# Kernel optimization log

Hardware: AMD Instinct MI355X
Metric: run time of the kernel (lower is better)

Reference implementation:

```python
import jax
import jax.numpy as jnp
from jax import lax
import numpy as np

IN_CH, HID, GROUPS = 1024, 256, 8
B, H, W = 16, 64, 64
CPG = HID // GROUPS  # channels per group = 32
EPS = 1e-5


def setup_inputs() -> dict:
    key = jax.random.key(0)
    ks = jax.random.split(key, 8)
    s = 0.02  # small init scale so activations stay well-behaved
    return {
        "x": jax.random.normal(ks[0], (B, IN_CH, H, W), jnp.float32),
        "ctx_w": jax.random.normal(ks[1], (HID, IN_CH), jnp.float32) * s,
        "ctx_b": jnp.zeros((HID,), jnp.float32),
        "kg_w1": jax.random.normal(ks[2], (2 * HID, HID), jnp.float32) * s,
        "kg_b1": jnp.zeros((2 * HID,), jnp.float32),
        "kg_w2": jax.random.normal(ks[3], (GROUPS * 9, 2 * HID), jnp.float32) * s,
        "kg_b2": jnp.zeros((GROUPS * 9,), jnp.float32),
        "in_w": jax.random.normal(ks[4], (HID, IN_CH), jnp.float32) * s,
        "in_b": jnp.zeros((HID,), jnp.float32),
        "out_w": jax.random.normal(ks[5], (HID, HID), jnp.float32) * s,
        "out_b": jnp.zeros((HID,), jnp.float32),
        "gamma": jnp.ones((HID,), jnp.float32),
        "beta": jnp.zeros((HID,), jnp.float32),
    }


def reference(x, ctx_w, ctx_b, kg_w1, kg_b1, kg_w2, kg_b2,
              in_w, in_b, out_w, out_b, gamma, beta):
    b = x.shape[0]
    # context pooling: global avg pool -> 1x1 conv -> relu
    ctx = jnp.mean(x, axis=(2, 3))                       # [B, C_in]
    ctx = jax.nn.relu(ctx @ ctx_w.T + ctx_b)             # [B, HID]
    # kernel generator MLP -> per-sample per-group 3x3 kernels
    hddn = jax.nn.relu(ctx @ kg_w1.T + kg_b1)            # [B, 2*HID]
    kernels = (hddn @ kg_w2.T + kg_b2).reshape(b, GROUPS, 3, 3)
    # input transform (1x1 conv)
    xt = jnp.einsum('bchw,oc->bohw', x, in_w) + in_b[None, :, None, None]
    # expand group kernels to per-channel depthwise kernels [B, HID, 3, 3]
    kch = jnp.repeat(kernels, CPG, axis=1)
    # per-sample depthwise 3x3 conv, padding=1
    def dwconv(xi, ki):  # xi: [HID, H, W], ki: [HID, 3, 3]
        return lax.conv_general_dilated(
            xi[None], ki[:, None], window_strides=(1, 1), padding='SAME',
            dimension_numbers=('NCHW', 'OIHW', 'NCHW'),
            feature_group_count=HID)[0]
    out = jax.vmap(dwconv)(xt, kch)                      # [B, HID, H, W]
    # output transform (1x1 conv)
    out = jnp.einsum('bchw,oc->bohw', out, out_w) + out_b[None, :, None, None]
    # BatchNorm2d (training-mode batch statistics)
    mean = jnp.mean(out, axis=(0, 2, 3))
    var = jnp.var(out, axis=(0, 2, 3))
    out = gamma[None, :, None, None] * (out - mean[None, :, None, None]) \
          * lax.rsqrt(var[None, :, None, None] + EPS) + beta[None, :, None, None]
    return xt + out
```

## Files before the change

kernel.cpp:

```cpp
#include <hip/hip_runtime.h>

#define BATCH 16
#define CIN   1024
#define HID   256
#define HW    4096

typedef __attribute__((ext_vector_type(8))) short bf16x8;
typedef __attribute__((ext_vector_type(4))) float f32x4;

struct __align__(16) f4  { float v[4]; };
struct __align__(8)  us4 { unsigned short v[4]; };
struct __align__(16) us8 { unsigned short v[8]; };

__device__ __forceinline__ float bf2f(unsigned short u) {
  unsigned int x = ((unsigned int)u) << 16;
  return __builtin_bit_cast(float, x);
}
__device__ __forceinline__ unsigned short f2bf(float f) {
  unsigned int u = __builtin_bit_cast(unsigned int, f);
  u += 0x7fff + ((u >> 16) & 1);
  return (unsigned short)(u >> 16);
}

#define LGWB() do { __builtin_amdgcn_sched_barrier(0); \
  asm volatile("s_waitcnt lgkmcnt(0)" ::: "memory"); \
  __builtin_amdgcn_s_barrier(); \
  __builtin_amdgcn_sched_barrier(0); } while (0)

__global__ __launch_bounds__(256)
void prep_kernel(const float* __restrict__ A1, unsigned short* __restrict__ O1,
                 const float* __restrict__ A2, unsigned short* __restrict__ O2,
                 float* __restrict__ zbuf)
{
  const int bidx = blockIdx.x;
  if (bidx >= 160) {
    int idx = (bidx - 160) * 256 + threadIdx.x;
    if (idx < 16896) zbuf[idx] = 0.f;
    return;
  }
  const float* A; unsigned short* O; int KD, u;
  if (bidx < 128) { A = A1; O = O1; KD = 1024; u = bidx * 256 + threadIdx.x; }
  else            { A = A2; O = O2; KD = 256;  u = (bidx - 128) * 256 + threadIdx.x; }
  const int t    = u >> 11;
  const int r    = u & 2047;
  const int wm   = r >> 9, kk = (r >> 8) & 1, mi = (r >> 6) & 3, lane = r & 63;
  const int row  = wm * 64 + mi * 16 + (lane & 15);
  const int k    = t * 64 + kk * 32 + (lane >> 4) * 8;
  f4 v0 = *(const f4*)(A + (size_t)row * KD + k);
  f4 v1 = *(const f4*)(A + (size_t)row * KD + k + 4);
  us8 w = { f2bf(v0.v[0]), f2bf(v0.v[1]), f2bf(v0.v[2]), f2bf(v0.v[3]),
            f2bf(v1.v[0]), f2bf(v1.v[1]), f2bf(v1.v[2]), f2bf(v1.v[3]) };
  *(us8*)(O + (size_t)u * 8) = w;
}

__global__ __launch_bounds__(512, 2)
void gemm1_kernel(const unsigned short* __restrict__ Afrag, const float* __restrict__ xb,
                  const float* __restrict__ bias, unsigned short* __restrict__ Cout,
                  float* __restrict__ ctx_sum)
{
  constexpr int NT = 16;
  __shared__ unsigned short B_sh[2][128 * 64];
  __shared__ float ctx_lds[1024];

  const int tid  = threadIdx.x;
  const int lane = tid & 63;
  const int wv   = tid >> 6;
  const int wm   = wv >> 1, wn = wv & 1;
  const int lr   = lane & 15, lg = lane >> 4;
  const int hi   = lane >> 5, q = lane & 31;

  const int b    = blockIdx.x >> 5;
  const int pix0 = (blockIdx.x & 31) << 7;

  for (int i = tid; i < 1024; i += 512) ctx_lds[i] = 0.f;
  __syncthreads();

  f32x4 acc[4][4] = {};
  const size_t rowbase = ((size_t)b * CIN + 8 * wv + hi) * HW + pix0 + 4 * q;
  const char*  abase   = (const char*)Afrag + wm * 8192 + lane * 16;

  bf16x8 aA[8], aB[8];
  f4 rfA[4], rfB[4];

  auto ISSUE_A = [&](int t, bf16x8* a) {
    const char* p = abase + t * 32768;
    #pragma unroll
    for (int i = 0; i < 8; ++i) a[i] = *(const bf16x8*)(p + i * 1024);
  };
  auto LOADB = [&](int t, f4* rf) {
    const float* p = xb + rowbase + (size_t)t * 64 * HW;
    #pragma unroll
    for (int i = 0; i < 4; ++i) rf[i] = *(const f4*)(p + (size_t)(2 * i) * HW);
  };
  auto WRITEB = [&](int sel, int t, f4* rf) {
    #pragma unroll
    for (int i = 0; i < 4; ++i) {
      float s = rf[i].v[0] + rf[i].v[1] + rf[i].v[2] + rf[i].v[3];
      #pragma unroll
      for (int m = 1; m < 32; m <<= 1) s += __shfl_xor(s, m, 64);
      if (q == 0) atomicAdd(&ctx_lds[t * 64 + 8 * wv + 2 * i + hi], s);
    }
    unsigned int u[4][2];
    #pragma unroll
    for (int i = 0; i < 4; ++i) {
      asm("v_cvt_pk_bf16_f32 %0, %1, %2" : "=v"(u[i][0]) : "v"(rf[i].v[0]), "v"(rf[i].v[1]));
      asm("v_cvt_pk_bf16_f32 %0, %1, %2" : "=v"(u[i][1]) : "v"(rf[i].v[2]), "v"(rf[i].v[3]));
    }
    unsigned int w[4][2];
    #pragma unroll
    for (int i = 0; i < 4; ++i) {
      w[i][0] = __shfl_xor(u[i][0], 32, 64);
      w[i][1] = __shfl_xor(u[i][1], 32, 64);
    }
    #pragma unroll
    for (int jj = 0; jj < 2; ++jj) {
      unsigned int A0 = hi ? w[2][jj] : u[0][jj];
      unsigned int A1 = hi ? u[2][jj] : w[0][jj];
      unsigned int A2 = hi ? w[3][jj] : u[1][jj];
      unsigned int A3 = hi ? u[3][jj] : w[1][jj];
      #pragma unroll
      for (int sub = 0; sub < 2; ++sub) {
        unsigned int lo, h2;
        if (sub == 0) { lo = (A0 & 0xffffu) | (A1 << 16);  h2 = (A2 & 0xffffu) | (A3 << 16); }
        else          { lo = (A0 >> 16) | (A1 & 0xffff0000u); h2 = (A2 >> 16) | (A3 & 0xffff0000u); }
        int p  = 4 * q + jj * 2 + sub;
        int fx = ((p >> 2) ^ p) & 7;
        int byte = p * 128 + (((wv ^ fx) & 7) << 4) + hi * 8;
        uint2 val; val.x = lo; val.y = h2;
        *(uint2*)((char*)B_sh[sel] + byte) = val;
      }
    }
  };
  auto COMPUTE = [&](int sel, bf16x8* a) {
    #pragma unroll
    for (int kk = 0; kk < 2; ++kk) {
      bf16x8 bfr[4];
      #pragma unroll
      for (int ni = 0; ni < 4; ++ni) {
        int pr = wn * 64 + ni * 16 + lr;
        int fx = ((pr >> 2) ^ pr) & 7;
        int byte = pr * 128 + ((((kk * 4 + lg) ^ fx) & 7) << 4);
        bfr[ni] = *(const bf16x8*)((const char*)B_sh[sel] + byte);
      }
      #pragma unroll
      for (int mi = 0; mi < 4; ++mi)
        #pragma unroll
        for (int ni = 0; ni < 4; ++ni)
          acc[mi][ni] = __builtin_amdgcn_mfma_f32_16x16x32_bf16(a[kk * 4 + mi], bfr[ni], acc[mi][ni], 0, 0, 0);
    }
  };

  ISSUE_A(0, aA);
  LOADB(0, rfA);
  LOADB(1, rfB);

  #pragma unroll
  for (int t = 0; t < NT; t += 2) {
    WRITEB(0, t, rfA);
    ISSUE_A(t + 1, aB);
    __builtin_amdgcn_sched_barrier(0);
    if (t + 2 < NT) LOADB(t + 2, rfA);
    LGWB();
    COMPUTE(0, aA);
    WRITEB(1, t + 1, rfB);
    if (t + 2 < NT) ISSUE_A(t + 2, aA);
    __builtin_amdgcn_sched_barrier(0);
    if (t + 3 < NT) LOADB(t + 3, rfB);
    LGWB();
    COMPUTE(1, aB);
  }

  #pragma unroll
  for (int mi = 0; mi < 4; ++mi) {
    #pragma unroll
    for (int r = 0; r < 4; ++r) {
      int o = wm * 64 + mi * 16 + lg * 4 + r;
      float bo = bias[o];
      #pragma unroll
      for (int ni = 0; ni < 4; ++ni) {
        int pix = pix0 + wn * 64 + ni * 16 + lr;
        Cout[((size_t)(b * HID + o)) * HW + pix] = f2bf(acc[mi][ni][r] + bo);
      }
    }
  }
  __syncthreads();
  for (int e = tid; e < 1024; e += 512)
    atomicAdd(&ctx_sum[(size_t)b * 1024 + e], ctx_lds[e]);
}

__global__ __launch_bounds__(512, 2)
void gemm2_fused_kernel(const unsigned short* __restrict__ Afrag,
                        const unsigned short* __restrict__ xt,
                        const float* __restrict__ kern, const float* __restrict__ bias,
                        unsigned short* __restrict__ Cout, float* __restrict__ bn_sums)
{
  constexpr int NT = 4;
  __shared__ unsigned short B_sh[128 * 64];
  __shared__ unsigned short xs[64 * 260];
  __shared__ float kf_s[72];
  __shared__ float bn_lds[512];

  const int tid  = threadIdx.x;
  const int lane = tid & 63;
  const int wv   = tid >> 6;
  const int wm   = wv >> 1, wn = wv & 1;
  const int lr   = lane & 15, lg = lane >> 4;

  const int b    = blockIdx.x >> 5;
  const int R    = blockIdx.x & 31;
  const int pix0 = R << 7;
  const int g0   = R << 1;

  if (tid < 512) bn_lds[tid] = 0.f;
  if (tid < 72)  kf_s[tid] = kern[b * 72 + tid];
  __syncthreads();

  f32x4 acc[4][4] = {};
  const int c4 = tid & 15, q = tid >> 4;
  const int prow  = q >> 4;
  const int pcol4 = (q & 15) << 2;
  const int grp9  = (c4 >> 3) * 9;

  const char* abase = (const char*)Afrag + wm * 8192 + lane * 16;

  bf16x8 aA[8];
  us8 rx[4];

  auto PREXS = [&](int t) {
    #pragma unroll
    for (int it = 0; it < 4; ++it) {
      int flat = it * 512 + tid;
      int ch = flat >> 5, r4 = (flat >> 3) & 3, c8 = flat & 7;
      int grow = g0 - 1 + r4;
      if ((unsigned)grow < 64u) {
        rx[it] = *(const us8*)(xt + ((size_t)(b * HID + t * 64 + ch) << 12) + grow * 64 + c8 * 8);
      } else {
        us8 z = {0, 0, 0, 0, 0, 0, 0, 0}; rx[it] = z;
      }
    }
  };
  auto WRXS = [&]() {
    #pragma unroll
    for (int it = 0; it < 4; ++it) {
      int flat = it * 512 + tid;
      int ch = flat >> 5, r4 = (flat >> 3) & 3, c8 = flat & 7;
      int o = ch * 260 + r4 * 64 + c8 * 8;
      *(us4*)(xs + o)     = *(const us4*)(&rx[it].v[0]);
      *(us4*)(xs + o + 4) = *(const us4*)(&rx[it].v[4]);
    }
  };
  auto ISSUE_A = [&](int t) {
    const char* p = abase + t * 32768;
    #pragma unroll
    for (int i = 0; i < 8; ++i) aA[i] = *(const bf16x8*)(p + i * 1024);
  };

  PREXS(0);
  ISSUE_A(0);

  for (int t = 0; t < NT; ++t) {
    WRXS();
    __syncthreads();
    if (t + 1 < NT) PREXS(t + 1);
    {
      const float k0 = kf_s[2 * t * 9 + grp9 + 0], k1 = kf_s[2 * t * 9 + grp9 + 1], k2 = kf_s[2 * t * 9 + grp9 + 2];
      const float k3 = kf_s[2 * t * 9 + grp9 + 3], k4 = kf_s[2 * t * 9 + grp9 + 4], k5 = kf_s[2 * t * 9 + grp9 + 5];
      const float k6 = kf_s[2 * t * 9 + grp9 + 6], k7 = kf_s[2 * t * 9 + grp9 + 7], k8 = kf_s[2 * t * 9 + grp9 + 8];
      float dwv[4][4];
      #pragma unroll
      for (int i = 0; i < 4; ++i) {
        int ch = 4 * c4 + i;
        #pragma unroll
        for (int j = 0; j < 4; ++j) dwv[i][j] = 0.f;
        #pragma unroll
        for (int ky = 0; ky < 3; ++ky) {
          int ro = ch * 260 + (prow + ky) * 64;
          float v[6];
          unsigned int p0 = (pcol4 > 0)  ? *(const unsigned int*)(xs + ro + pcol4 - 2) : 0u;
          unsigned int p1 = *(const unsigned int*)(xs + ro + pcol4);
          unsigned int p2 = *(const unsigned int*)(xs + ro + pcol4 + 2);
          unsigned int p3 = (pcol4 < 60) ? *(const unsigned int*)(xs + ro + pcol4 + 4) : 0u;
          v[0] = bf2f((unsigned short)(p0 >> 16));
          v[1] = bf2f((unsigned short)(p1 & 0xffff));
          v[2] = bf2f((unsigned short)(p1 >> 16));
          v[3] = bf2f((unsigned short)(p2 & 0xffff));
          v[4] = bf2f((unsigned short)(p2 >> 16));
          v[5] = bf2f((unsigned short)(p3 & 0xffff));
          float ka = (ky == 0) ? k0 : (ky == 1) ? k3 : k6;
          float kb = (ky == 0) ? k1 : (ky == 1) ? k4 : k7;
          float kc = (ky == 0) ? k2 : (ky == 1) ? k5 : k8;
          #pragma unroll
          for (int j = 0; j < 4; ++j)
            dwv[i][j] += v[j] * ka + v[j + 1] * kb + v[j + 2] * kc;
        }
      }
      #pragma unroll
      for (int j = 0; j < 4; ++j) {
        int pix = 4 * q + j;
        us4 w = { f2bf(dwv[0][j]), f2bf(dwv[1][j]), f2bf(dwv[2][j]), f2bf(dwv[3][j]) };
        *(us4*)((char*)B_sh + pix * 128 + ((8 * c4) ^ ((pix & 7) << 4))) = w;
      }
    }
    __syncthreads();
    #pragma unroll
    for (int kk = 0; kk < 2; ++kk) {
      bf16x8 bfr[4];
      #pragma unroll
      for (int ni = 0; ni < 4; ++ni) {
        int pr = wn * 64 + ni * 16 + lr;
        bfr[ni] = *(const bf16x8*)((const char*)B_sh + pr * 128 + ((((kk << 2) | lg) ^ (pr & 7)) << 4));
      }
      #pragma unroll
      for (int mi = 0; mi < 4; ++mi)
        #pragma unroll
        for (int ni = 0; ni < 4; ++ni)
          acc[mi][ni] = __builtin_amdgcn_mfma_f32_16x16x32_bf16(aA[kk * 4 + mi], bfr[ni], acc[mi][ni], 0, 0, 0);
    }
    if (t + 1 < NT) ISSUE_A(t + 1);
  }

  #pragma unroll
  for (int mi = 0; mi < 4; ++mi) {
    #pragma unroll
    for (int r = 0; r < 4; ++r) {
      int o = wm * 64 + mi * 16 + lg * 4 + r;
      float bo = bias[o];
      float s = 0.f, s2 = 0.f;
      #pragma unroll
      for (int ni = 0; ni < 4; ++ni) {
        int pix = pix0 + wn * 64 + ni * 16 + lr;
        float val = acc[mi][ni][r] + bo;
        Cout[((size_t)(b * HID + o)) * HW + pix] = f2bf(val);
        s += val; s2 += val * val;
      }
      #pragma unroll
      for (int msk = 1; msk < 16; msk <<= 1) {
        s  += __shfl_xor(s,  msk, 64);
        s2 += __shfl_xor(s2, msk, 64);
      }
      if (lr == 0) { atomicAdd(&bn_lds[o], s); atomicAdd(&bn_lds[256 + o], s2); }
    }
  }
  __syncthreads();
  if (tid < 512) atomicAdd(&bn_sums[tid], bn_lds[tid]);
}

template<int K, int N, bool RELU>
__global__ __launch_bounds__(256)
void fc_kernel(const float* __restrict__ in, const float* __restrict__ w,
               const float* __restrict__ bias, float* __restrict__ out, float scale)
{
  const int wid  = (blockIdx.x << 2) | (threadIdx.x >> 6);
  const int lane = threadIdx.x & 63;
  const int b = wid / N, o = wid - b * N;
  const float* ip = in + (size_t)b * K;
  const float* wp = w  + (size_t)o * K;
  float p = 0.f;
  #pragma unroll
  for (int k = 0; k < K / 64; ++k) p += ip[lane + k * 64] * wp[lane + k * 64];
  #pragma unroll
  for (int m = 1; m < 64; m <<= 1) p += __shfl_xor(p, m, 64);
  if (lane == 0) {
    float v = p * scale + bias[o];
    out[(size_t)b * N + o] = RELU ? fmaxf(v, 0.f) : v;
  }
}

__global__ __launch_bounds__(256)
void final_kernel(const unsigned short* __restrict__ xt, const unsigned short* __restrict__ ot,
                  const float* __restrict__ bn_sums, const float* __restrict__ gamma,
                  const float* __restrict__ beta, float* __restrict__ out)
{
  __shared__ float sc_s[256], sh_s[256];
  {
    int t = threadIdx.x;
    const float inv_n = 1.f / 65536.f;
    float m  = bn_sums[t] * inv_n;
    float v  = bn_sums[256 + t] * inv_n - m * m;
    float sc = gamma[t] * rsqrtf(v + 1e-5f);
    sc_s[t] = sc;
    sh_s[t] = beta[t] - m * sc;
  }
  __syncthreads();
  int g = blockIdx.x * 256 + threadIdx.x;
  const int stride = 4096 * 256;
  #pragma unroll
  for (int it = 0; it < 4; ++it, g += stride) {
    int o = (g >> 10) & 255;
    us4 a = ((const us4*)xt)[g];
    us4 c = ((const us4*)ot)[g];
    float s = sc_s[o], h = sh_s[o];
    f4 r;
    #pragma unroll
    for (int j = 0; j < 4; ++j) r.v[j] = bf2f(a.v[j]) + s * bf2f(c.v[j]) + h;
    *(f4*)(out + (size_t)g * 4) = r;
  }
}

extern "C" void kernel_launch(void* const* d_in, const int* in_sizes, int n_in,
                              void* d_out, int out_size, void* d_ws, size_t ws_size,
                              hipStream_t stream)
{
  const float* x     = (const float*)d_in[0];
  const float* ctx_w = (const float*)d_in[1];
  const float* ctx_b = (const float*)d_in[2];
  const float* kg_w1 = (const float*)d_in[3];
  const float* kg_b1 = (const float*)d_in[4];
  const float* kg_w2 = (const float*)d_in[5];
  const float* kg_b2 = (const float*)d_in[6];
  const float* in_w  = (const float*)d_in[7];
  const float* in_b  = (const float*)d_in[8];
  const float* out_w = (const float*)d_in[9];
  const float* out_b = (const float*)d_in[10];
  const float* gamma = (const float*)d_in[11];
  const float* beta  = (const float*)d_in[12];
  float* out = (float*)d_out;

  char* ws = (char*)d_ws;
  unsigned short* xt = (unsigned short*)ws;
  unsigned short* ot = (unsigned short*)(ws + 33554432);
  float* ctx_sum = (float*)(ws + 67108864);
  float* bn_sums = ctx_sum + 16384;
  float* kern    = bn_sums + 512;
  float* ctxbuf  = kern + 1152;
  float* hddnbuf = ctxbuf + 4096;
  unsigned short* afrag1 = (unsigned short*)(ws + 67108864 + 131072);
  unsigned short* afrag2 = (unsigned short*)(ws + 67108864 + 131072 + 524288);

  prep_kernel<<<226, 256, 0, stream>>>(in_w, afrag1, out_w, afrag2, ctx_sum);
  gemm1_kernel<<<512, 512, 0, stream>>>(afrag1, x, in_b, xt, ctx_sum);
  fc_kernel<1024, 256, true ><<<1024, 256, 0, stream>>>(ctx_sum, ctx_w, ctx_b, ctxbuf, 1.f / 4096.f);
  fc_kernel< 256, 512, true ><<<2048, 256, 0, stream>>>(ctxbuf,  kg_w1, kg_b1, hddnbuf, 1.f);
  fc_kernel< 512,  72, false><<< 288, 256, 0, stream>>>(hddnbuf, kg_w2, kg_b2, kern,    1.f);
  gemm2_fused_kernel<<<512, 512, 0, stream>>>(afrag2, xt, kern, out_b, ot, bn_sums);
  final_kernel<<<4096, 256, 0, stream>>>(xt, ot, bn_sums, gamma, beta, out);
}
```

Measured before the change: 165.0 us.

## Deepen gemm1 prefetch, lighten gemm2 barriers, fuse kernel-generator MLP launches

gemm1 now cycles three register buffers for x tiles, so each tile is loaded three steps ahead instead of two. The loop is fully unrolled through a STEP helper that alternates the A-fragment and LDS buffers. In gemm2, the two __syncthreads per iteration are replaced by the LGWB macro, a scheduled wait-plus-barrier, so outstanding loads can overlap the barrier better. The two kernel-generator fc launches are merged into one kg_kernel with one block per sample and the hidden layer kept in LDS. This removes a launch and an intermediate buffer, but the fused stage now runs on only 16 blocks and uses more registers.

```diff
diff --git a/kernel.cpp b/kernel.cpp
--- a/kernel.cpp
+++ b/kernel.cpp
@@ -80,7 +80,7 @@
   const char*  abase   = (const char*)Afrag + wm * 8192 + lane * 16;
 
   bf16x8 aA[8], aB[8];
-  f4 rfA[4], rfB[4];
+  f4 rfA[4], rfB[4], rfC[4];
 
   auto ISSUE_A = [&](int t, bf16x8* a) {
     const char* p = abase + t * 32768;
@@ -149,26 +149,26 @@
           acc[mi][ni] = __builtin_amdgcn_mfma_f32_16x16x32_bf16(a[kk * 4 + mi], bfr[ni], acc[mi][ni], 0, 0, 0);
     }
   };
+  auto STEP = [&](int t, f4* rfc, bf16x8* ac, bf16x8* an) {
+    WRITEB(t & 1, t, rfc);
+    if (t + 1 < NT) ISSUE_A(t + 1, an);
+    __builtin_amdgcn_sched_barrier(0);
+    if (t + 3 < NT) LOADB(t + 3, rfc);
+    LGWB();
+    COMPUTE(t & 1, ac);
+  };
 
   ISSUE_A(0, aA);
   LOADB(0, rfA);
   LOADB(1, rfB);
-
-  #pragma unroll
-  for (int t = 0; t < NT; t += 2) {
-    WRITEB(0, t, rfA);
-    ISSUE_A(t + 1, aB);
-    __builtin_amdgcn_sched_barrier(0);
-    if (t + 2 < NT) LOADB(t + 2, rfA);
-    LGWB();
-    COMPUTE(0, aA);
-    WRITEB(1, t + 1, rfB);
-    if (t + 2 < NT) ISSUE_A(t + 2, aA);
-    __builtin_amdgcn_sched_barrier(0);
-    if (t + 3 < NT) LOADB(t + 3, rfB);
-    LGWB();
-    COMPUTE(1, aB);
-  }
+  LOADB(2, rfC);
+
+  STEP( 0, rfA, aA, aB);  STEP( 1, rfB, aB, aA);  STEP( 2, rfC, aA, aB);
+  STEP( 3, rfA, aB, aA);  STEP( 4, rfB, aA, aB);  STEP( 5, rfC, aB, aA);
+  STEP( 6, rfA, aA, aB);  STEP( 7, rfB, aB, aA);  STEP( 8, rfC, aA, aB);
+  STEP( 9, rfA, aB, aA);  STEP(10, rfB, aA, aB);  STEP(11, rfC, aB, aA);
+  STEP(12, rfA, aA, aB);  STEP(13, rfB, aB, aA);  STEP(14, rfC, aA, aB);
+  STEP(15, rfA, aB, aA);
 
   #pragma unroll
   for (int mi = 0; mi < 4; ++mi) {
@@ -260,7 +260,7 @@
 
   for (int t = 0; t < NT; ++t) {
     WRXS();
-    __syncthreads();
+    LGWB();
     if (t + 1 < NT) PREXS(t + 1);
     {
       const float k0 = kf_s[2 * t * 9 + grp9 + 0], k1 = kf_s[2 * t * 9 + grp9 + 1], k2 = kf_s[2 * t * 9 + grp9 + 2];
@@ -301,7 +301,7 @@
         *(us4*)((char*)B_sh + pix * 128 + ((8 * c4) ^ ((pix & 7) << 4))) = w;
       }
     }
-    __syncthreads();
+    LGWB();
     #pragma unroll
     for (int kk = 0; kk < 2; ++kk) {
       bf16x8 bfr[4];
@@ -363,6 +363,38 @@
   if (lane == 0) {
     float v = p * scale + bias[o];
     out[(size_t)b * N + o] = RELU ? fmaxf(v, 0.f) : v;
+  }
+}
+
+__global__ __launch_bounds__(512)
+void kg_kernel(const float* __restrict__ ctxbuf, const float* __restrict__ kg_w1,
+               const float* __restrict__ kg_b1, const float* __restrict__ kg_w2,
+               const float* __restrict__ kg_b2, float* __restrict__ kern)
+{
+  __shared__ float ctx_s[256];
+  __shared__ float hdn_s[512];
+  const int b = blockIdx.x, tid = threadIdx.x, lane = tid & 63, wv = tid >> 6;
+  if (tid < 256) ctx_s[tid] = ctxbuf[b * 256 + tid];
+  __syncthreads();
+  #pragma unroll 4
+  for (int j = wv * 64; j < wv * 64 + 64; ++j) {
+    const float* wp = kg_w1 + (size_t)j * 256;
+    float p = 0.f;
+    #pragma unroll
+    for (int k = 0; k < 4; ++k) p += ctx_s[lane + k * 64] * wp[lane + k * 64];
+    #pragma unroll
+    for (int m = 1; m < 64; m <<= 1) p += __shfl_xor(p, m, 64);
+    if (lane == 0) hdn_s[j] = fmaxf(p + kg_b1[j], 0.f);
+  }
+  __syncthreads();
+  for (int j = wv; j < 72; j += 8) {
+    const float* wp = kg_w2 + (size_t)j * 512;
+    float p = 0.f;
+    #pragma unroll
+    for (int k = 0; k < 8; ++k) p += hdn_s[lane + k * 64] * wp[lane + k * 64];
+    #pragma unroll
+    for (int m = 1; m < 64; m <<= 1) p += __shfl_xor(p, m, 64);
+    if (lane == 0) kern[b * 72 + j] = p + kg_b2[j];
   }
 }
 
@@ -423,15 +455,13 @@
   float* bn_sums = ctx_sum + 16384;
   float* kern    = bn_sums + 512;
   float* ctxbuf  = kern + 1152;
-  float* hddnbuf = ctxbuf + 4096;
   unsigned short* afrag1 = (unsigned short*)(ws + 67108864 + 131072);
   unsigned short* afrag2 = (unsigned short*)(ws + 67108864 + 131072 + 524288);
 
   prep_kernel<<<226, 256, 0, stream>>>(in_w, afrag1, out_w, afrag2, ctx_sum);
   gemm1_kernel<<<512, 512, 0, stream>>>(afrag1, x, in_b, xt, ctx_sum);
-  fc_kernel<1024, 256, true ><<<1024, 256, 0, stream>>>(ctx_sum, ctx_w, ctx_b, ctxbuf, 1.f / 4096.f);
-  fc_kernel< 256, 512, true ><<<2048, 256, 0, stream>>>(ctxbuf,  kg_w1, kg_b1, hddnbuf, 1.f);
-  fc_kernel< 512,  72, false><<< 288, 256, 0, stream>>>(hddnbuf, kg_w2, kg_b2, kern,    1.f);
+  fc_kernel<1024, 256, true><<<1024, 256, 0, stream>>>(ctx_sum, ctx_w, ctx_b, ctxbuf, 1.f / 4096.f);
+  kg_kernel<<<16, 512, 0, stream>>>(ctxbuf, kg_w1, kg_b1, kg_w2, kg_b2, kern);
   gemm2_fused_kernel<<<512, 512, 0, stream>>>(afrag2, xt, kern, out_b, ot, bn_sums);
   final_kernel<<<4096, 256, 0, stream>>>(xt, ot, bn_sums, gamma, beta, out);
 }
```

Result: slower. 220.8 us (+33.8%).
